# Performance work log

Hardware: AMD Instinct MI355X
Metric: run time of the kernel (lower is better)

## Reference

```python
import jax, jax.numpy as jnp
import numpy as np

P, F_IN, HG, C, T, E, HOUT = 4096, 64, 64, 64, 32, 65536, 12
LEAKY_SLOPE = 0.2
LN_EPS = 1e-5


def setup_inputs() -> dict:
    key = jax.random.key(0)
    ks = jax.random.split(key, 14)
    g = lambda k, shape, scale: (jax.random.normal(k, shape, jnp.float32) * scale)
    return {
        "X": jax.random.normal(ks[0], (1, P, F_IN, T), jnp.float32),
        "edge_index": jax.random.randint(ks[1], (T, 2, E), 0, P, jnp.int32),
        # GATv2 params (single head)
        "Wl": g(ks[2], (F_IN, HG), 0.1),
        "Wr": g(ks[3], (F_IN, HG), 0.1),
        "att": g(ks[4], (HG,), 0.1),
        "gat_b": g(ks[5], (HG,), 0.02),
        # 1x1 time conv (HG -> C) and 1x1 residual conv (F_IN -> C)
        "W_time": g(ks[6], (C, HG), 0.1),
        "b_time": g(ks[7], (C,), 0.02),
        "W_res": g(ks[8], (C, F_IN), 0.1),
        "b_res": g(ks[9], (C,), 0.02),
        # LayerNorm over channel dim C
        "ln_g": jnp.ones((C,), jnp.float32),
        "ln_b": jnp.zeros((C,), jnp.float32),
        # final conv: Conv2d(in=T, out=HOUT, kernel=(1, C)) -> weight (HOUT, T, C)
        "W_final": g(ks[10], (HOUT, T, C), 0.05),
        "b_final": g(ks[11], (HOUT,), 0.02),
    }


def reference(X, edge_index, Wl, Wr, att, gat_b, W_time, b_time, W_res, b_res,
              ln_g, ln_b, W_final, b_final):
    Pn = X.shape[1]

    def gat_t(x, edges):
        # x: (P, F_IN), edges: (2, E) with edges[0]=src j, edges[1]=dst i
        src, dst = edges[0], edges[1]
        hl = x @ Wl                      # (P, HG) messages
        hr = x @ Wr                      # (P, HG) query side
        e = jax.nn.leaky_relu(hl[src] + hr[dst], LEAKY_SLOPE) @ att  # (E,)
        emax = jax.ops.segment_max(e, dst, num_segments=Pn)
        ex = jnp.exp(e - emax[dst])
        den = jax.ops.segment_sum(ex, dst, num_segments=Pn)
        alpha = ex / den[dst]            # softmax over in-edges of each dst
        return jax.ops.segment_sum(alpha[:, None] * hl[src], dst,
                                   num_segments=Pn) + gat_b  # (P, HG)

    xs = jnp.moveaxis(X[0], -1, 0)                     # (T, P, F_IN)
    X_hat = jax.nn.relu(jax.vmap(gat_t)(xs, edge_index))  # (T, P, HG)

    th = jnp.einsum('tph,ch->tpc', X_hat, W_time) + b_time  # time conv 1x1
    rs = jnp.einsum('tpf,cf->tpc', xs, W_res) + b_res       # residual conv 1x1
    y = jax.nn.relu(th + rs)                                 # (T, P, C)

    mu = jnp.mean(y, axis=-1, keepdims=True)
    var = jnp.var(y, axis=-1, keepdims=True)
    yn = (y - mu) * jax.lax.rsqrt(var + LN_EPS) * ln_g + ln_b  # (T, P, C)

    # final conv: in-channels = T, kernel (1, C) -> contract over t and c
    out = jnp.einsum('tpc,otc->po', yn, W_final) + b_final     # (P, HOUT)
    return out[None]                                           # (1, P, HOUT)
```

## Files before the change

kernel.cpp:

```cpp
#include <hip/hip_runtime.h>
#include <math.h>

#define NP 4096
#define F_IN 64
#define HG 64
#define NC 64
#define NT 32
#define NE 65536
#define HOUT 12
#define LEAKY 0.2f
#define LN_EPS 1e-5f
#define CAPC 32

template <int CTRL>
__device__ __forceinline__ float dppadd(float v, float x) {
    int r = __builtin_amdgcn_update_dpp(0, __builtin_bit_cast(int, x), CTRL, 0xF, 0xF, false);
    return v + __builtin_bit_cast(float, r);
}
__device__ __forceinline__ float rowsum16(float v) {
    v = dppadd<0x128>(v, v);
    v = dppadd<0x124>(v, v);
    v = dppadd<0x122>(v, v);
    v = dppadd<0x121>(v, v);
    return v;
}
__device__ __forceinline__ float laneXorSum(float v) {
    v += __shfl_xor(v, 16, 64);
    v += __shfl_xor(v, 32, 64);
    return v;
}

#define FMA4(Acomp, B, r)                                                     \
    acc[r][0] += (Acomp) * (B).x; acc[r][1] += (Acomp) * (B).y;               \
    acc[r][2] += (Acomp) * (B).z; acc[r][3] += (Acomp) * (B).w;

__global__ __launch_bounds__(256) void k_front(const float* __restrict__ X,
        const float* __restrict__ Wl, const float* __restrict__ Wr,
        const float* __restrict__ W_res, const float* __restrict__ b_res,
        const float* __restrict__ W_time, const float* __restrict__ bf,
        const int* __restrict__ EI,
        float* __restrict__ hl, float* __restrict__ hr, float* __restrict__ rs,
        float* __restrict__ wtT, float* __restrict__ out,
        int* __restrict__ cnt, unsigned short* __restrict__ scap) {
    __shared__ float smem[8960];
    int b = blockIdx.x;
    int tid = threadIdx.x;
    if (b < 512) {
        unsigned short (*buck)[CAPC] = (unsigned short (*)[CAPC])smem;
        int* cnts = (int*)(smem + 8192);
        int t = (b & 7) + 8 * ((b >> 3) & 3);
        int rem = b >> 5;
        int c = rem & 1, r = rem >> 1;
        cnts[tid] = 0; cnts[tid + 256] = 0;
        __syncthreads();
        const int4* srcA = (const int4*)(EI + (size_t)t * 2 * NE) + c * (NE / 8);
        const int4* dstA = (const int4*)(EI + (size_t)t * 2 * NE + NE) + c * (NE / 8);
        for (int i = tid; i < NE / 8; i += 256) {
            int4 s = srcA[i];
            int4 d = dstA[i];
            if ((d.x >> 9) == r) { int lo = d.x & 511; int sl = atomicAdd(&cnts[lo], 1); if (sl < CAPC) buck[lo][sl] = (unsigned short)s.x; }
            if ((d.y >> 9) == r) { int lo = d.y & 511; int sl = atomicAdd(&cnts[lo], 1); if (sl < CAPC) buck[lo][sl] = (unsigned short)s.y; }
            if ((d.z >> 9) == r) { int lo = d.z & 511; int sl = atomicAdd(&cnts[lo], 1); if (sl < CAPC) buck[lo][sl] = (unsigned short)s.z; }
            if ((d.w >> 9) == r) { int lo = d.w & 511; int sl = atomicAdd(&cnts[lo], 1); if (sl < CAPC) buck[lo][sl] = (unsigned short)s.w; }
        }
        __syncthreads();
        int obase = ((t * 2 + c) << 12) + (r << 9);
        cnt[obase + tid] = cnts[tid];
        cnt[obase + tid + 256] = cnts[tid + 256];
        unsigned int* dstw = (unsigned int*)(scap + (size_t)obase * CAPC);
        const unsigned int* srcw = (const unsigned int*)buck;
        for (int i = tid; i < 512 * CAPC / 2; i += 256)
            dstw[i] = srcw[i];
    } else if (b < 2560) {
        float (*xs)[F_IN][36] = (float (*)[F_IN][36])smem;
        float (*bk)[68] = (float (*)[68])(smem + 4608);
        int p0 = (b - 512) * 2;
        const float4* Xp = (const float4*)(X + (size_t)p0 * F_IN * NT);
        for (int i4 = tid; i4 < 1024; i4 += 256) {
            int pp = i4 >> 9, f = (i4 >> 3) & 63, t0 = (i4 & 7) * 4;
            *(float4*)&xs[pp][f][t0] = Xp[i4];
        }
        int ng = tid & 15, pp = (tid >> 4) & 1, tg = tid >> 5;
        int n0 = ng * 4, t0 = tg * 4;
        {
            const float4* B4 = (const float4*)Wl;
            for (int i4 = tid; i4 < 1024; i4 += 256)
                *(float4*)&bk[i4 >> 4][(i4 & 15) * 4] = B4[i4];
            __syncthreads();
            float acc[4][4];
#pragma unroll
            for (int i = 0; i < 4; ++i)
#pragma unroll
                for (int j2 = 0; j2 < 4; ++j2) acc[i][j2] = 0.f;
#pragma unroll 8
            for (int f = 0; f < F_IN; ++f) {
                float4 B = *(const float4*)&bk[f][n0];
                float4 A = *(const float4*)&xs[pp][f][t0];
                FMA4(A.x, B, 0) FMA4(A.y, B, 1) FMA4(A.z, B, 2) FMA4(A.w, B, 3)
            }
#pragma unroll
            for (int i = 0; i < 4; ++i) {
                float4 v;
                v.x = acc[i][0]; v.y = acc[i][1]; v.z = acc[i][2]; v.w = acc[i][3];
                *(float4*)&hl[((size_t)(t0 + i) * NP + p0 + pp) * HG + n0] = v;
            }
            __syncthreads();
        }
        {
            const float4* B4 = (const float4*)Wr;
            for (int i4 = tid; i4 < 1024; i4 += 256)
                *(float4*)&bk[i4 >> 4][(i4 & 15) * 4] = B4[i4];
            __syncthreads();
            float acc[4][4];
#pragma unroll
            for (int i = 0; i < 4; ++i)
#pragma unroll
                for (int j2 = 0; j2 < 4; ++j2) acc[i][j2] = 0.f;
#pragma unroll 8
            for (int f = 0; f < F_IN; ++f) {
                float4 B = *(const float4*)&bk[f][n0];
                float4 A = *(const float4*)&xs[pp][f][t0];
                FMA4(A.x, B, 0) FMA4(A.y, B, 1) FMA4(A.z, B, 2) FMA4(A.w, B, 3)
            }
#pragma unroll
            for (int i = 0; i < 4; ++i) {
                float4 v;
                v.x = acc[i][0]; v.y = acc[i][1]; v.z = acc[i][2]; v.w = acc[i][3];
                *(float4*)&hr[((size_t)(t0 + i) * NP + p0 + pp) * HG + n0] = v;
            }
            __syncthreads();
        }
        {
            for (int i = tid; i < F_IN * NC; i += 256) {
                int c = i >> 6, f = i & 63;
                bk[f][c] = W_res[i];
            }
            __syncthreads();
            float4 br4 = *(const float4*)&b_res[n0];
            float acc[4][4];
#pragma unroll
            for (int i = 0; i < 4; ++i) {
                acc[i][0] = br4.x; acc[i][1] = br4.y; acc[i][2] = br4.z; acc[i][3] = br4.w;
            }
#pragma unroll 8
            for (int f = 0; f < F_IN; ++f) {
                float4 B = *(const float4*)&bk[f][n0];
                float4 A = *(const float4*)&xs[pp][f][t0];
                FMA4(A.x, B, 0) FMA4(A.y, B, 1) FMA4(A.z, B, 2) FMA4(A.w, B, 3)
            }
#pragma unroll
            for (int i = 0; i < 4; ++i) {
                float4 v;
                v.x = acc[i][0]; v.y = acc[i][1]; v.z = acc[i][2]; v.w = acc[i][3];
                *(float4*)&rs[((size_t)(t0 + i) * NP + p0 + pp) * NC + n0] = v;
            }
        }
    } else if (b < 2576) {
        int i = (b - 2560) * 256 + tid;
        wtT[i] = W_time[(i & 63) * 64 + (i >> 6)];
    } else {
        int i = (b - 2576) * 256 + tid;
        out[i] = bf[i % HOUT];
    }
}

__global__ __launch_bounds__(256) void k_gat(const float* __restrict__ hl,
        float* __restrict__ hr,
        const int* __restrict__ cnt, const unsigned short* __restrict__ scap,
        const float* __restrict__ att, const float* __restrict__ gat_b) {
    __shared__ int sidx[4][64];
    int b = blockIdx.x;
    int k = b >> 3;
    int t = (b & 7) + 8 * (k >> 10);
    int ws = threadIdx.x >> 6;
    int i = (k & 1023) * 4 + ws;
    int lane = threadIdx.x & 63;
    int row = lane >> 4;
    int c0 = (lane & 15) * 4;
    size_t nbase = ((size_t)t * NP + i) * HG;
    const float* hlt = hl + (size_t)t * NP * HG;
    float4 r4 = *(const float4*)&hr[nbase + c0];
    float4 at4 = *(const float4*)&att[c0];
    int d0 = cnt[((t * 2 + 0) << 12) + i]; d0 = (d0 < CAPC) ? d0 : CAPC;
    int d1 = cnt[((t * 2 + 1) << 12) + i]; d1 = (d1 < CAPC) ? d1 : CAPC;
    int deg = d0 + d1;
    deg = (deg < 64) ? deg : 64;
    const unsigned short* s0 = scap + ((size_t)(((t * 2 + 0) << 12) + i)) * CAPC;
    const unsigned short* s1 = scap + ((size_t)(((t * 2 + 1) << 12) + i)) * CAPC;
    int li = (lane < deg) ? lane : 0;
    int f1 = (li >= d0);
    int idx = f1 ? (li - d0) : li;
    sidx[ws][lane] = (int)(f1 ? s1 : s0)[idx];
    float l = 0.f;
    float4 acc = {0.f, 0.f, 0.f, 0.f};
    int nfull = deg & ~7;
    int j = 0;
    for (; j < nfull; j += 8) {
        int src0 = sidx[ws][j + row];
        int src1 = sidx[ws][j + 4 + row];
        float4 h0 = *(const float4*)&hlt[((size_t)src0 << 6) + c0];
        float4 h1 = *(const float4*)&hlt[((size_t)src1 << 6) + c0];
        float4 z0, z1;
        z0.x = h0.x + r4.x; z0.y = h0.y + r4.y; z0.z = h0.z + r4.z; z0.w = h0.w + r4.w;
        z1.x = h1.x + r4.x; z1.y = h1.y + r4.y; z1.z = h1.z + r4.z; z1.w = h1.w + r4.w;
        z0.x = fmaxf(z0.x, LEAKY * z0.x); z0.y = fmaxf(z0.y, LEAKY * z0.y);
        z0.z = fmaxf(z0.z, LEAKY * z0.z); z0.w = fmaxf(z0.w, LEAKY * z0.w);
        z1.x = fmaxf(z1.x, LEAKY * z1.x); z1.y = fmaxf(z1.y, LEAKY * z1.y);
        z1.z = fmaxf(z1.z, LEAKY * z1.z); z1.w = fmaxf(z1.w, LEAKY * z1.w);
        float e0 = rowsum16(z0.x * at4.x + z0.y * at4.y + z0.z * at4.z + z0.w * at4.w);
        float e1 = rowsum16(z1.x * at4.x + z1.y * at4.y + z1.z * at4.z + z1.w * at4.w);
        float w0 = __expf(e0);
        float w1 = __expf(e1);
        l += w0 + w1;
        acc.x += w0 * h0.x + w1 * h1.x;
        acc.y += w0 * h0.y + w1 * h1.y;
        acc.z += w0 * h0.z + w1 * h1.z;
        acc.w += w0 * h0.w + w1 * h1.w;
    }
    for (; j < deg; j += 4) {
        int jj = j + row;
        int src = sidx[ws][(jj < deg) ? jj : 0];
        float4 ha = *(const float4*)&hlt[((size_t)src << 6) + c0];
        float4 za;
        za.x = ha.x + r4.x; za.y = ha.y + r4.y; za.z = ha.z + r4.z; za.w = ha.w + r4.w;
        za.x = fmaxf(za.x, LEAKY * za.x);
        za.y = fmaxf(za.y, LEAKY * za.y);
        za.z = fmaxf(za.z, LEAKY * za.z);
        za.w = fmaxf(za.w, LEAKY * za.w);
        float ep = za.x * at4.x + za.y * at4.y + za.z * at4.z + za.w * at4.w;
        float e = rowsum16(ep);
        float w = __expf(e);
        w = (jj < deg) ? w : 0.f;
        l += w;
        acc.x += w * ha.x; acc.y += w * ha.y; acc.z += w * ha.z; acc.w += w * ha.w;
    }
    float lt = laneXorSum(l);
    acc.x = laneXorSum(acc.x);
    acc.y = laneXorSum(acc.y);
    acc.z = laneXorSum(acc.z);
    acc.w = laneXorSum(acc.w);
    if (row == 0) {
        float inv = (deg > 0) ? (1.0f / lt) : 0.f;
        float4 gb = *(const float4*)&gat_b[c0];
        float4 o;
        o.x = fmaxf(acc.x * inv + gb.x, 0.f);
        o.y = fmaxf(acc.y * inv + gb.y, 0.f);
        o.z = fmaxf(acc.z * inv + gb.z, 0.f);
        o.w = fmaxf(acc.w * inv + gb.w, 0.f);
        *(float4*)&hr[nbase + c0] = o;
    }
}

__global__ __launch_bounds__(256) void k_pf(const float* __restrict__ Xhat,
        const float* __restrict__ wtT, const float* __restrict__ b_time,
        const float* __restrict__ rs, const float* __restrict__ ln_g,
        const float* __restrict__ ln_b, const float* __restrict__ Wf,
        float* __restrict__ out) {
    __shared__ float in_t[64][68];
    __shared__ float bk[64][68];
    int bx = blockIdx.x;
    int tc = bx & 15;
    int p0 = (bx >> 4) * 64;
    int tid = threadIdx.x;
    const float4* wsrc = (const float4*)wtT;
    for (int i4 = tid; i4 < 1024; i4 += 256) {
        int h = i4 >> 4, c4 = (i4 & 15) * 4;
        *(float4*)&bk[h][c4] = wsrc[i4];
    }
    int cg = tid & 15, pg = tid >> 4;
    int c0 = cg * 4, pl = pg * 4;
    float4 bt4 = *(const float4*)&b_time[c0];
    float4 lg = *(const float4*)&ln_g[c0];
    float4 lb = *(const float4*)&ln_b[c0];
    float ot[4][HOUT];
#pragma unroll
    for (int i = 0; i < 4; ++i)
#pragma unroll
        for (int o = 0; o < HOUT; ++o) ot[i][o] = 0.f;
    for (int ti = 0; ti < 2; ++ti) {
        int t = tc + ti * 16;
        __syncthreads();
        const float4* src = (const float4*)(Xhat + ((size_t)t * NP + p0) * HG);
        for (int i4 = tid; i4 < 1024; i4 += 256) {
            int pp = i4 >> 4, c4 = (i4 & 15) * 4;
            *(float4*)&in_t[pp][c4] = src[i4];
        }
        __syncthreads();
        float acc[4][4];
#pragma unroll
        for (int i = 0; i < 4; ++i) {
            acc[i][0] = bt4.x; acc[i][1] = bt4.y; acc[i][2] = bt4.z; acc[i][3] = bt4.w;
        }
#pragma unroll
        for (int k4 = 0; k4 < 16; ++k4) {
            float4 A0 = *(const float4*)&in_t[pl + 0][k4 * 4];
            float4 A1 = *(const float4*)&in_t[pl + 1][k4 * 4];
            float4 A2 = *(const float4*)&in_t[pl + 2][k4 * 4];
            float4 A3 = *(const float4*)&in_t[pl + 3][k4 * 4];
            float4 B0 = *(const float4*)&bk[k4 * 4 + 0][c0];
            FMA4(A0.x, B0, 0) FMA4(A1.x, B0, 1) FMA4(A2.x, B0, 2) FMA4(A3.x, B0, 3)
            float4 B1 = *(const float4*)&bk[k4 * 4 + 1][c0];
            FMA4(A0.y, B1, 0) FMA4(A1.y, B1, 1) FMA4(A2.y, B1, 2) FMA4(A3.y, B1, 3)
            float4 B2 = *(const float4*)&bk[k4 * 4 + 2][c0];
            FMA4(A0.z, B2, 0) FMA4(A1.z, B2, 1) FMA4(A2.z, B2, 2) FMA4(A3.z, B2, 3)
            float4 B3 = *(const float4*)&bk[k4 * 4 + 3][c0];
            FMA4(A0.w, B3, 0) FMA4(A1.w, B3, 1) FMA4(A2.w, B3, 2) FMA4(A3.w, B3, 3)
        }
        float4 ynv[4];
#pragma unroll
        for (int i = 0; i < 4; ++i) {
            size_t prow = (size_t)t * NP + p0 + pl + i;
            float4 r4 = *(const float4*)&rs[prow * NC + c0];
            float y0 = fmaxf(acc[i][0] + r4.x, 0.f), y1 = fmaxf(acc[i][1] + r4.y, 0.f);
            float y2 = fmaxf(acc[i][2] + r4.z, 0.f), y3 = fmaxf(acc[i][3] + r4.w, 0.f);
            float s = rowsum16(y0 + y1 + y2 + y3);
            float ss = rowsum16(y0 * y0 + y1 * y1 + y2 * y2 + y3 * y3);
            float mu = s * (1.f / 64.f);
            float var = ss * (1.f / 64.f) - mu * mu;
            float rsd = rsqrtf(var + LN_EPS);
            ynv[i].x = (y0 - mu) * rsd * lg.x + lb.x;
            ynv[i].y = (y1 - mu) * rsd * lg.y + lb.y;
            ynv[i].z = (y2 - mu) * rsd * lg.z + lb.z;
            ynv[i].w = (y3 - mu) * rsd * lg.w + lb.w;
        }
#pragma unroll
        for (int o = 0; o < HOUT; ++o) {
            float4 w4 = *(const float4*)&Wf[(size_t)o * NT * NC + t * NC + c0];
#pragma unroll
            for (int i = 0; i < 4; ++i)
                ot[i][o] += ynv[i].x * w4.x + ynv[i].y * w4.y
                          + ynv[i].z * w4.z + ynv[i].w * w4.w;
        }
    }
#pragma unroll
    for (int i = 0; i < 4; ++i)
#pragma unroll
        for (int o = 0; o < HOUT; ++o) ot[i][o] = rowsum16(ot[i][o]);
    if (cg == 0) {
#pragma unroll
        for (int i = 0; i < 4; ++i) {
            int p = p0 + pl + i;
#pragma unroll
            for (int o = 0; o < HOUT; ++o)
                atomicAdd(&out[p * HOUT + o], ot[i][o]);
        }
    }
}

extern "C" void kernel_launch(void* const* d_in, const int* in_sizes, int n_in,
                              void* d_out, int out_size, void* d_ws, size_t ws_size,
                              hipStream_t stream) {
    const float* X      = (const float*)d_in[0];
    const int*   EI     = (const int*)d_in[1];
    const float* Wl     = (const float*)d_in[2];
    const float* Wr     = (const float*)d_in[3];
    const float* att    = (const float*)d_in[4];
    const float* gat_b  = (const float*)d_in[5];
    const float* W_time = (const float*)d_in[6];
    const float* b_time = (const float*)d_in[7];
    const float* W_res  = (const float*)d_in[8];
    const float* b_res  = (const float*)d_in[9];
    const float* ln_g   = (const float*)d_in[10];
    const float* ln_b   = (const float*)d_in[11];
    const float* Wf     = (const float*)d_in[12];
    const float* bf     = (const float*)d_in[13];
    float* out = (float*)d_out;

    char* ws = (char*)d_ws;
    const size_t MB = 1024 * 1024;
    float* hl   = (float*)(ws);
    float* hr   = (float*)(ws + 32 * MB);
    float* rs   = (float*)(ws + 64 * MB);
    float* wtT  = (float*)(ws + 96 * MB);
    int*   cnt  = (int*)  (ws + 97 * MB);
    unsigned short* scap = (unsigned short*)(ws + 98 * MB);

    k_front<<<2768, 256, 0, stream>>>(X, Wl, Wr, W_res, b_res, W_time, bf, EI,
                                      hl, hr, rs, wtT, out, cnt, scap);
    k_gat  <<<(NT * NP) / 4, 256, 0, stream>>>(hl, hr, cnt, scap, att, gat_b);
    k_pf   <<<1024, 256, 0, stream>>>(hr, wtT, b_time, rs, ln_g, ln_b, Wf, out);
}
```

Measured before the change: 285.3 us.

## Prefetch gathers in GAT loop, register double-buffer k_pf, drop W_time transpose blocks

The GAT aggregation loop now prefetches the next pair of neighbor rows while computing the current ones. It pads the index list and masks tail weights instead of running a separate remainder loop, and adds an occupancy hint and a uniform wave index. k_pf now processes four time steps per block with register prefetch of the next Xhat tile, halving the grid, and transposes W_time directly into shared memory. This removes the separate transpose blocks from k_front. The xs shared-memory padding also changes to reduce bank conflicts. Risks are extra wasted gathers on padded edges, a strided uncoalesced W_time load, and fewer blocks in k_pf.

```diff
diff --git a/kernel.cpp b/kernel.cpp
--- a/kernel.cpp
+++ b/kernel.cpp
@@ -37,12 +37,12 @@
 __global__ __launch_bounds__(256) void k_front(const float* __restrict__ X,
         const float* __restrict__ Wl, const float* __restrict__ Wr,
         const float* __restrict__ W_res, const float* __restrict__ b_res,
-        const float* __restrict__ W_time, const float* __restrict__ bf,
+        const float* __restrict__ bf,
         const int* __restrict__ EI,
         float* __restrict__ hl, float* __restrict__ hr, float* __restrict__ rs,
-        float* __restrict__ wtT, float* __restrict__ out,
+        float* __restrict__ out,
         int* __restrict__ cnt, unsigned short* __restrict__ scap) {
-    __shared__ float smem[8960];
+    __shared__ float smem[9472];
     int b = blockIdx.x;
     int tid = threadIdx.x;
     if (b < 512) {
@@ -72,8 +72,8 @@
         for (int i = tid; i < 512 * CAPC / 2; i += 256)
             dstw[i] = srcw[i];
     } else if (b < 2560) {
-        float (*xs)[F_IN][36] = (float (*)[F_IN][36])smem;
-        float (*bk)[68] = (float (*)[68])(smem + 4608);
+        float (*xs)[F_IN][40] = (float (*)[F_IN][40])smem;
+        float (*bk)[68] = (float (*)[68])(smem + 5120);
         int p0 = (b - 512) * 2;
         const float4* Xp = (const float4*)(X + (size_t)p0 * F_IN * NT);
         for (int i4 = tid; i4 < 1024; i4 += 256) {
@@ -155,51 +155,54 @@
                 *(float4*)&rs[((size_t)(t0 + i) * NP + p0 + pp) * NC + n0] = v;
             }
         }
-    } else if (b < 2576) {
+    } else {
         int i = (b - 2560) * 256 + tid;
-        wtT[i] = W_time[(i & 63) * 64 + (i >> 6)];
-    } else {
-        int i = (b - 2576) * 256 + tid;
         out[i] = bf[i % HOUT];
     }
 }
 
-__global__ __launch_bounds__(256) void k_gat(const float* __restrict__ hl,
+__global__ __launch_bounds__(256, 8) void k_gat(const float* __restrict__ hl,
         float* __restrict__ hr,
         const int* __restrict__ cnt, const unsigned short* __restrict__ scap,
         const float* __restrict__ att, const float* __restrict__ gat_b) {
-    __shared__ int sidx[4][64];
+    __shared__ int sidx[4][72];
     int b = blockIdx.x;
     int k = b >> 3;
     int t = (b & 7) + 8 * (k >> 10);
-    int ws = threadIdx.x >> 6;
+    int ws = __builtin_amdgcn_readfirstlane(threadIdx.x >> 6);
     int i = (k & 1023) * 4 + ws;
     int lane = threadIdx.x & 63;
     int row = lane >> 4;
     int c0 = (lane & 15) * 4;
-    size_t nbase = ((size_t)t * NP + i) * HG;
     const float* hlt = hl + (size_t)t * NP * HG;
-    float4 r4 = *(const float4*)&hr[nbase + c0];
     float4 at4 = *(const float4*)&att[c0];
     int d0 = cnt[((t * 2 + 0) << 12) + i]; d0 = (d0 < CAPC) ? d0 : CAPC;
     int d1 = cnt[((t * 2 + 1) << 12) + i]; d1 = (d1 < CAPC) ? d1 : CAPC;
     int deg = d0 + d1;
-    deg = (deg < 64) ? deg : 64;
-    const unsigned short* s0 = scap + ((size_t)(((t * 2 + 0) << 12) + i)) * CAPC;
-    const unsigned short* s1 = scap + ((size_t)(((t * 2 + 1) << 12) + i)) * CAPC;
+    const unsigned short* s0p = scap + ((size_t)(((t * 2 + 0) << 12) + i)) * CAPC;
+    const unsigned short* s1p = scap + ((size_t)(((t * 2 + 1) << 12) + i)) * CAPC;
     int li = (lane < deg) ? lane : 0;
     int f1 = (li >= d0);
     int idx = f1 ? (li - d0) : li;
-    sidx[ws][lane] = (int)(f1 ? s1 : s0)[idx];
+    sidx[ws][lane] = (int)(f1 ? s1p : s0p)[idx];
+    if (lane < 8) sidx[ws][64 + lane] = 0;
+    size_t nbase = ((size_t)t * NP + i) * HG;
+    float4 r4 = *(const float4*)&hr[nbase + c0];
+    int degp = (deg + 7) & ~7;
     float l = 0.f;
     float4 acc = {0.f, 0.f, 0.f, 0.f};
-    int nfull = deg & ~7;
-    int j = 0;
-    for (; j < nfull; j += 8) {
-        int src0 = sidx[ws][j + row];
-        int src1 = sidx[ws][j + 4 + row];
-        float4 h0 = *(const float4*)&hlt[((size_t)src0 << 6) + c0];
-        float4 h1 = *(const float4*)&hlt[((size_t)src1 << 6) + c0];
+    float4 h0, h1;
+    {
+        int sa = sidx[ws][row];
+        int sb = sidx[ws][4 + row];
+        h0 = *(const float4*)&hlt[((size_t)sa << 6) + c0];
+        h1 = *(const float4*)&hlt[((size_t)sb << 6) + c0];
+    }
+    for (int j = 0; j < degp; j += 8) {
+        int na = sidx[ws][j + 8 + row];
+        int nb = sidx[ws][j + 12 + row];
+        float4 hn0 = *(const float4*)&hlt[((size_t)na << 6) + c0];
+        float4 hn1 = *(const float4*)&hlt[((size_t)nb << 6) + c0];
         float4 z0, z1;
         z0.x = h0.x + r4.x; z0.y = h0.y + r4.y; z0.z = h0.z + r4.z; z0.w = h0.w + r4.w;
         z1.x = h1.x + r4.x; z1.y = h1.y + r4.y; z1.z = h1.z + r4.z; z1.w = h1.w + r4.w;
@@ -211,28 +214,14 @@
         float e1 = rowsum16(z1.x * at4.x + z1.y * at4.y + z1.z * at4.z + z1.w * at4.w);
         float w0 = __expf(e0);
         float w1 = __expf(e1);
+        w0 = (j + row < deg) ? w0 : 0.f;
+        w1 = (j + 4 + row < deg) ? w1 : 0.f;
         l += w0 + w1;
         acc.x += w0 * h0.x + w1 * h1.x;
         acc.y += w0 * h0.y + w1 * h1.y;
         acc.z += w0 * h0.z + w1 * h1.z;
         acc.w += w0 * h0.w + w1 * h1.w;
-    }
-    for (; j < deg; j += 4) {
-        int jj = j + row;
-        int src = sidx[ws][(jj < deg) ? jj : 0];
-        float4 ha = *(const float4*)&hlt[((size_t)src << 6) + c0];
-        float4 za;
-        za.x = ha.x + r4.x; za.y = ha.y + r4.y; za.z = ha.z + r4.z; za.w = ha.w + r4.w;
-        za.x = fmaxf(za.x, LEAKY * za.x);
-        za.y = fmaxf(za.y, LEAKY * za.y);
-        za.z = fmaxf(za.z, LEAKY * za.z);
-        za.w = fmaxf(za.w, LEAKY * za.w);
-        float ep = za.x * at4.x + za.y * at4.y + za.z * at4.z + za.w * at4.w;
-        float e = rowsum16(ep);
-        float w = __expf(e);
-        w = (jj < deg) ? w : 0.f;
-        l += w;
-        acc.x += w * ha.x; acc.y += w * ha.y; acc.z += w * ha.z; acc.w += w * ha.w;
+        h0 = hn0; h1 = hn1;
     }
     float lt = laneXorSum(l);
     acc.x = laneXorSum(acc.x);
@@ -252,21 +241,18 @@
 }
 
 __global__ __launch_bounds__(256) void k_pf(const float* __restrict__ Xhat,
-        const float* __restrict__ wtT, const float* __restrict__ b_time,
+        const float* __restrict__ W_time, const float* __restrict__ b_time,
         const float* __restrict__ rs, const float* __restrict__ ln_g,
         const float* __restrict__ ln_b, const float* __restrict__ Wf,
         float* __restrict__ out) {
     __shared__ float in_t[64][68];
     __shared__ float bk[64][68];
     int bx = blockIdx.x;
-    int tc = bx & 15;
-    int p0 = (bx >> 4) * 64;
+    int tc = bx & 7;
+    int p0 = (bx >> 3) * 64;
     int tid = threadIdx.x;
-    const float4* wsrc = (const float4*)wtT;
-    for (int i4 = tid; i4 < 1024; i4 += 256) {
-        int h = i4 >> 4, c4 = (i4 & 15) * 4;
-        *(float4*)&bk[h][c4] = wsrc[i4];
-    }
+    for (int i = tid; i < 4096; i += 256)
+        bk[i & 63][i >> 6] = W_time[i];
     int cg = tid & 15, pg = tid >> 4;
     int c0 = cg * 4, pl = pg * 4;
     float4 bt4 = *(const float4*)&b_time[c0];
@@ -277,15 +263,26 @@
     for (int i = 0; i < 4; ++i)
 #pragma unroll
         for (int o = 0; o < HOUT; ++o) ot[i][o] = 0.f;
-    for (int ti = 0; ti < 2; ++ti) {
-        int t = tc + ti * 16;
+    float4 rg[4];
+    {
+        const float4* src = (const float4*)(Xhat + ((size_t)tc * NP + p0) * HG);
+#pragma unroll
+        for (int r = 0; r < 4; ++r) rg[r] = src[tid + 256 * r];
+    }
+    for (int ti = 0; ti < 4; ++ti) {
+        int t = tc + ti * 8;
         __syncthreads();
-        const float4* src = (const float4*)(Xhat + ((size_t)t * NP + p0) * HG);
-        for (int i4 = tid; i4 < 1024; i4 += 256) {
-            int pp = i4 >> 4, c4 = (i4 & 15) * 4;
-            *(float4*)&in_t[pp][c4] = src[i4];
+#pragma unroll
+        for (int r = 0; r < 4; ++r) {
+            int i4 = tid + 256 * r;
+            *(float4*)&in_t[i4 >> 4][(i4 & 15) * 4] = rg[r];
         }
         __syncthreads();
+        if (ti < 3) {
+            const float4* src = (const float4*)(Xhat + ((size_t)(t + 8) * NP + p0) * HG);
+#pragma unroll
+            for (int r = 0; r < 4; ++r) rg[r] = src[tid + 256 * r];
+        }
         float acc[4][4];
 #pragma unroll
         for (int i = 0; i < 4; ++i) {
@@ -371,12 +368,11 @@
     float* hl   = (float*)(ws);
     float* hr   = (float*)(ws + 32 * MB);
     float* rs   = (float*)(ws + 64 * MB);
-    float* wtT  = (float*)(ws + 96 * MB);
-    int*   cnt  = (int*)  (ws + 97 * MB);
-    unsigned short* scap = (unsigned short*)(ws + 98 * MB);
-
-    k_front<<<2768, 256, 0, stream>>>(X, Wl, Wr, W_res, b_res, W_time, bf, EI,
-                                      hl, hr, rs, wtT, out, cnt, scap);
+    int*   cnt  = (int*)  (ws + 96 * MB);
+    unsigned short* scap = (unsigned short*)(ws + 97 * MB);
+
+    k_front<<<2752, 256, 0, stream>>>(X, Wl, Wr, W_res, b_res, bf, EI,
+                                      hl, hr, rs, out, cnt, scap);
     k_gat  <<<(NT * NP) / 4, 256, 0, stream>>>(hl, hr, cnt, scap, att, gat_b);
-    k_pf   <<<1024, 256, 0, stream>>>(hr, wtT, b_time, rs, ln_g, ln_b, Wf, out);
-}
+    k_pf   <<<512, 256, 0, stream>>>(hr, W_time, b_time, rs, ln_g, ln_b, Wf, out);
+}
```

Measured after the change: 271.7 us. 1.05x faster.
